# Kernel optimization log

Hardware: AMD Instinct MI355X
Metric: run time of the kernel (lower is better)

The kernel has to match this reference:

```python
import jax, jax.numpy as jnp
import numpy as np

NEG_SLOPE = 0.01  # torch LeakyReLU default
EPS = 1e-5        # torch BatchNorm2d default
N_BINS = 17       # quantization indices 0..16 for uniform [0,1) input


def _bn(x, g, b):
    # training-mode BatchNorm2d: biased batch stats over (B, H, W) per channel
    m = jnp.mean(x, axis=(0, 2, 3), keepdims=True)
    v = jnp.var(x, axis=(0, 2, 3), keepdims=True)
    return (x - m) * jax.lax.rsqrt(v + EPS) * g[None, :, None, None] + b[None, :, None, None]


def _lrelu(x):
    return jnp.where(x >= 0, x, NEG_SLOPE * x)


def _mode_pool_11(idx):
    # idx: int32 (B,C,H,W) quantization bin indices; 11x11 reflect-padded sliding-window mode.
    # Histogram formulation: one-hot over N_BINS, box-sum via 2D integral image, argmax.
    # argmax takes the FIRST max -> smallest modal value, matching torch.mode tie-breaking.
    k = jnp.pad(idx, ((0, 0), (0, 0), (5, 5), (5, 5)), mode='reflect')
    oh = (k[..., None] == jnp.arange(N_BINS, dtype=jnp.int32)).astype(jnp.float32)  # (B,C,Hp,Wp,17)
    I = jnp.cumsum(jnp.cumsum(oh, axis=2), axis=3)
    I = jnp.pad(I, ((0, 0), (0, 0), (1, 0), (1, 0), (0, 0)))
    cnt = I[:, :, 11:, 11:] - I[:, :, :-11, 11:] - I[:, :, 11:, :-11] + I[:, :, :-11, :-11]
    return jnp.argmax(cnt, axis=-1)  # (B,C,H,W) int


def _nearest(x, H, W):
    # torch F.interpolate mode='nearest': src = floor(dst * in / out)
    h, w = x.shape[2], x.shape[3]
    ri = (jnp.arange(H) * h) // H
    ci = (jnp.arange(W) * w) // W
    return x[:, :, ri][:, :, :, ci]


def _conv1x1(x, w, b):
    return jnp.einsum('bchw,oc->bohw', x, w) + b[None, :, None, None]


def reference(x, pw1, pb1, g1, be1, pw2, pb2, g2, be2, dw, sw, gs, bs):
    B, C, H, W = x.shape
    half = pw1.shape[0]
    # quantize: (x*255/16).round() * 16/256 -> index path (round has zero grad anyway)
    idx = jnp.round(x * 255.0 / 16.0).astype(jnp.int32)
    xq = _mode_pool_11(idx).astype(x.dtype) * (16.0 / 256.0)
    # prepare: conv1x1 -> BN -> LeakyReLU, twice
    h1 = _lrelu(_bn(_conv1x1(xq, pw1, pb1), g1, be1))
    prep = _lrelu(_bn(_conv1x1(h1, pw2, pb2), g2, be2))
    score = jnp.zeros((B, 2 * half, H, W), dtype=x.dtype)
    dn = ('NCHW', 'OIHW', 'NCHW')
    previous = prep
    d = prep
    # static pyramid: 512 -> 171 -> 57 -> 19 -> 7 -> 3 -> 1 (shapes known at trace time)
    while min(d.shape[2], d.shape[3]) >= 3:
        d = jax.lax.conv_general_dilated(d, dw, (3, 3), ((1, 1), (1, 1)), dimension_numbers=dn)
        z = _nearest(d, H, W)
        # interleave previous/zoomout per channel: ch 2c=prev[c], 2c+1=zoom[c]
        mix = jnp.stack([previous, z], axis=2).reshape(B, 2 * half, H, W)
        previous = z
        # grouped 1x1 conv: groups=half, 2 in / 2 out channels per group, no bias
        sc = jnp.einsum('bgihw,goi->bgohw', mix.reshape(B, half, 2, H, W), sw).reshape(B, 2 * half, H, W)
        score = score + _lrelu(_bn(sc, gs, bs))
    return score


def setup_inputs() -> dict:
    key = jax.random.key(0)
    ks = jax.random.split(key, 6)
    B, C, H, W = 8, 3, 512, 512
    half = 16
    x = jax.random.uniform(ks[0], (B, C, H, W), dtype=jnp.float32)
    pw1 = 0.1 * jax.random.normal(ks[1], (half, C), dtype=jnp.float32)
    pb1 = jnp.zeros((half,), jnp.float32)
    g1 = jnp.ones((half,), jnp.float32)
    be1 = jnp.zeros((half,), jnp.float32)
    pw2 = 0.1 * jax.random.normal(ks[2], (half, half), dtype=jnp.float32)
    pb2 = jnp.zeros((half,), jnp.float32)
    g2 = jnp.ones((half,), jnp.float32)
    be2 = jnp.zeros((half,), jnp.float32)
    dw = 0.1 * jax.random.normal(ks[3], (half, half, 3, 3), dtype=jnp.float32)
    sw = 0.1 * jax.random.normal(ks[4], (half, 2, 2), dtype=jnp.float32)
    gs = jnp.ones((2 * half,), jnp.float32)
    bs = jnp.zeros((2 * half,), jnp.float32)
    return {'x': x, 'pw1': pw1, 'pb1': pb1, 'g1': g1, 'be1': be1,
            'pw2': pw2, 'pb2': pb2, 'g2': g2, 'be2': be2,
            'dw': dw, 'sw': sw, 'gs': gs, 'bs': bs}
```

## Files before the change

kernel.cpp:

```cpp
#include <hip/hip_runtime.h>
#include <stdint.h>


#define NPX   2097152
#define NINV  (1.0f/2097152.0f)

#define OFF_STATS 0
#define OFF_HIST  16384
#define OFF_LUT   36864
#define OFF_MODE  194560
#define OFF_D1    73594880
#define OFF_D2    88566272
#define OFF_D3    90229760
#define OFF_D4    90414592
#define OFF_D5    90439680
#define OFF_D6    90444288

#define S_PRE1    0
#define S2_PRE1   16
#define S_H1      32
#define S_H1H1    48
#define S_PREP    184
#define S2_PREP   200
#define S_Z1      216
// ... 7 lines not shown
#define P_AFF     848

__device__ __forceinline__ uint32_t f2bf(float f) {
  uint32_t u = __float_as_uint(f);
  u += 0x7FFFu + ((u >> 16) & 1u);
  return u >> 16;
}
__device__ __forceinline__ float bf2f(uint32_t u) {
  return __uint_as_float(u << 16);
}

__device__ __forceinline__ float wave_red(float v) {
  v += __shfl_down(v, 32); v += __shfl_down(v, 16); v += __shfl_down(v, 8);
  v += __shfl_down(v, 4);  v += __shfl_down(v, 2);  v += __shfl_down(v, 1);
  return v;
}

template<int K, bool ATOMIC>
__device__ __forceinline__ void block_red(float* acc, float* dst, float* lds) {
  int lane = threadIdx.x & 63, wid = threadIdx.x >> 6;
#pragma unroll
  for (int k = 0; k < K; ++k) {
    float v = wave_red(acc[k]);
    if (lane == 0) lds[wid * K + k] = v;
  }
  __syncthreads();
  if ((int)threadIdx.x < K) {
    float s = lds[threadIdx.x] + lds[K + threadIdx.x] + lds[2 * K + threadIdx.x] + lds[3 * K + threadIdx.x];
    if (ATOMIC) atomicAdd(&dst[threadIdx.x], s);
    else        dst[threadIdx.x] = s;
  }
}

__global__ __launch_bounds__(256) void k_mode(const float* __restrict__ x,
                                              uint8_t* __restrict__ mode) {
  int bx = blockIdx.x;
  int rb = bx & 15, cb = (bx >> 4) & 1, pl = bx >> 5;
  __shared__ uint8_t tile[42][272];
  const float* xp = x + (size_t)pl * 262144;
  int tid = threadIdx.x;
  for (int e = tid; e < 42 * 266; e += 256) {
    int lr = e / 266, lc = e - lr * 266;
    int gr = rb * 32 - 5 + lr; if (gr < 0) gr = -gr; else if (gr > 511) gr = 1022 - gr;
    int gc = cb * 256 - 5 + lc; if (gc < 0) gc = -gc; else if (gc > 511) gc = 1022 - gc;
    float v = xp[gr * 512 + gc];
    tile[lr][lc] = (uint8_t)(int)rintf((v * 255.0f) * 0.0625f);
  }
  __syncthreads();
  int t = tid;
  uint32_t h0 = 0, h1 = 0, h2 = 0, h3 = 0, h4 = 0;
#define ADDV(vv) { int v_ = (vv); uint32_t inc_ = 1u << ((v_ & 3) << 3); int w_ = v_ >> 2; \
    h0 += (w_ == 0) ? inc_ : 0u; h1 += (w_ == 1) ? inc_ : 0u; h2 += (w_ == 2) ? inc_ : 0u; \
    h3 += (w_ == 3) ? inc_ : 0u; h4 += (w_ == 4) ? inc_ : 0u; }
#define SUBV(vv) { int v_ = (vv); uint32_t inc_ = 1u << ((v_ & 3) << 3); int w_ = v_ >> 2; \
    h0 -= (w_ == 0) ? inc_ : 0u; h1 -= (w_ == 1) ? inc_ : 0u; h2 -= (w_ == 2) ? inc_ : 0u; \
    h3 -= (w_ == 3) ? inc_ : 0u; h4 -= (w_ == 4) ? inc_ : 0u; }
#define SCAN_STORE(OI) { uint32_t best_ = h0 & 255u; int bi_ = 0; uint32_t c_; \
    c_ = (h0 >> 8)  & 255u; if (c_ > best_) { best_ = c_; bi_ = 1; } \
    c_ = (h0 >> 16) & 255u; if (c_ > best_) { best_ = c_; bi_ = 2; } \
    c_ = (h0 >> 24);        if (c_ > best_) { best_ = c_; bi_ = 3; } \
    c_ = h1 & 255u;         if (c_ > best_) { best_ = c_; bi_ = 4; } \
    c_ = (h1 >> 8)  & 255u; if (c_ > best_) { best_ = c_; bi_ = 5; } \
    c_ = (h1 >> 16) & 255u; if (c_ > best_) { best_ = c_; bi_ = 6; } \
    c_ = (h1 >> 24);        if (c_ > best_) { best_ = c_; bi_ = 7; } \
    c_ = h2 & 255u;         if (c_ > best_) { best_ = c_; bi_ = 8; } \
    c_ = (h2 >> 8)  & 255u; if (c_ > best_) { best_ = c_; bi_ = 9; } \
    c_ = (h2 >> 16) & 255u; if (c_ > best_) { best_ = c_; bi_ = 10; } \
    c_ = (h2 >> 24);        if (c_ > best_) { best_ = c_; bi_ = 11; } \
    c_ = h3 & 255u;         if (c_ > best_) { best_ = c_; bi_ = 12; } \
    c_ = (h3 >> 8)  & 255u; if (c_ > best_) { best_ = c_; bi_ = 13; } \
    c_ = (h3 >> 16) & 255u; if (c_ > best_) { best_ = c_; bi_ = 14; } \
    c_ = (h3 >> 24);        if (c_ > best_) { best_ = c_; bi_ = 15; } \
    c_ = h4 & 255u;         if (c_ > best_) { best_ = c_; bi_ = 16; } \
    mode[OI] = (uint8_t)bi_; }
#pragma unroll
  for (int dy = 0; dy < 11; ++dy) {
#pragma unroll
    for (int dx = 0; dx < 11; ++dx) ADDV(tile[dy][t + dx]);
  }
  size_t ob = (size_t)pl * 262144 + (size_t)(rb * 32) * 512 + cb * 256 + t;
  SCAN_STORE(ob);
  for (int s = 1; s < 32; ++s) {
#pragma unroll
    for (int dx = 0; dx < 11; ++dx) { SUBV(tile[s - 1][t + dx]); ADDV(tile[s + 10][t + dx]); }
    SCAN_STORE(ob + (size_t)s * 512);
  }
#undef ADDV
#undef SUBV
#undef SCAN_STORE
}

__global__ __launch_bounds__(256) void k_hist(const uint8_t* __restrict__ mode,
                                              uint32_t* __restrict__ hist) {
  __shared__ uint32_t h[4913];
  int tid = threadIdx.x;
  for (int e = tid; e < 4913; e += 256) h[e] = 0;
  __syncthreads();
  int base = blockIdx.x * 8192;
  for (int it = 0; it < 16; ++it) {
    int px = base + it * 512 + tid * 2;
    int b = px >> 18, rem = px & 262143;
    const uint8_t* mp = mode + (size_t)b * 786432 + rem;
    uint32_t m0 = *(const uint16_t*)(mp);
    uint32_t m1 = *(const uint16_t*)(mp + 262144);
    uint32_t m2 = *(const uint16_t*)(mp + 524288);
    int c0 = (int)(m0 & 255u) + 17 * (int)(m1 & 255u) + 289 * (int)(m2 & 255u);
    int c1 = (int)(m0 >> 8)   + 17 * (int)(m1 >> 8)   + 289 * (int)(m2 >> 8);
    atomicAdd(&h[c0], 1u);
    atomicAdd(&h[c1], 1u);
  }
  __syncthreads();
  for (int e = tid; e < 4913; e += 256)
    if (h[e]) atomicAdd(&hist[e], h[e]);
}

__global__ __launch_bounds__(256) void k_build(const uint32_t* __restrict__ hist,
    const float* __restrict__ pw1, const float* __restrict__ pb1,
    const float* __restrict__ g1,  const float* __restrict__ be1,
    const float* __restrict__ pw2, const float* __restrict__ pb2,
    const float* __restrict__ g2,  const float* __restrict__ be2,
    float* __restrict__ stats, uint32_t* __restrict__ lut) {
  __shared__ float red[4 * 152];
  int tid = threadIdx.x;
  {
    float acc[32];
#pragma unroll
    for (int k = 0; k < 32; ++k) acc[k] = 0.f;
    for (int bin = tid; bin < 4913; bin += 256) {
      float w = (float)hist[bin];
      if (w == 0.f) continue;
      int m0 = bin % 17, r = bin / 17;
      int m1 = r % 17, m2 = r / 17;
      float x0 = m0 * 0.0625f, x1 = m1 * 0.0625f, x2 = m2 * 0.0625f;
#pragma unroll
      for (int o = 0; o < 16; ++o) {
        float p = fmaf(pw1[o * 3], x0, fmaf(pw1[o * 3 + 1], x1, fmaf(pw1[o * 3 + 2], x2, pb1[o])));
        acc[o] = fmaf(w, p, acc[o]);
        acc[16 + o] = fmaf(w * p, p, acc[16 + o]);
      }
    }
    block_red<32, false>(acc, stats + S_PRE1, red);
  }
  __syncthreads();
  if (tid < 16) {
    int o = tid;
    float m = stats[S_PRE1 + o] * NINV;
// ... 62 lines not shown
    float acc[32];
#pragma unroll
    for (int k = 0; k < 32; ++k) acc[k] = 0.f;
    for (int bin = tid; bin < 4913; bin += 256) {
      float w = (float)hist[bin];
      int m0 = bin % 17, r = bin / 17;
      int m1 = r % 17, m2 = r / 17;
      float x0 = m0 * 0.0625f, x1 = m1 * 0.0625f, x2 = m2 * 0.0625f;
      float h[16];
#pragma unroll
      for (int c = 0; c < 16; ++c) {
        float y = fmaf(stats[P_A1 + c * 3], x0, fmaf(stats[P_A1 + c * 3 + 1], x1,
                  fmaf(stats[P_A1 + c * 3 + 2], x2, stats[P_B1 + c])));
        h[c] = fmaxf(y, 0.01f * y);
      }
      float p[16];
#pragma unroll
      for (int o = 0; o < 16; ++o) {
        float y = stats[P_B2 + o];
#pragma unroll
        for (int c = 0; c < 16; ++c) y = fmaf(stats[P_A2 + o * 16 + c], h[c], y);
        p[o] = fmaxf(y, 0.01f * y);
        acc[o] = fmaf(w, p[o], acc[o]);
        acc[16 + o] = fmaf(w * p[o], p[o], acc[16 + o]);
      }
#pragma unroll
      for (int d = 0; d < 8; ++d)
        lut[bin * 8 + d] = f2bf(p[2 * d]) | (f2bf(p[2 * d + 1]) << 16);
    }
    block_red<32, false>(acc, stats + S_PREP, red);
  }
}

template<int HIN, int WIN, int HOUT, int WOUT>
__device__ __forceinline__ void conv_body(const float* __restrict__ in,
                                          float* __restrict__ out,
                                          const float* __restrict__ dw, int bx) {
  __shared__ float tile[3][16][WIN + 2];
  int r = bx % HOUT, b = bx / HOUT;
  int tid = threadIdx.x;
  for (int e = tid; e < 48; e += 256) { tile[e / 16][e & 15][0] = 0.f; tile[e / 16][e & 15][WIN + 1] = 0.f; }
  for (int e = tid; e < 3 * 16 * WIN; e += 256) {
    int ky = e / (16 * WIN); int rem = e - ky * (16 * WIN); int ic = rem / WIN; int col = rem - ic * WIN;
    int gr = 3 * r - 1 + ky;
    float v = 0.f;
    if (gr >= 0 && gr < HIN) v = in[((size_t)(b * 16 + ic) * HIN + gr) * WIN + col];
    tile[ky][ic][col + 1] = v;
  }
  __syncthreads();
  int c = tid;
  if (c < WOUT) {
    float acc[16];
#pragma unroll
    for (int o = 0; o < 16; ++o) acc[o] = 0.f;
#pragma unroll
    for (int ic = 0; ic < 16; ++ic) {
      float v[9];
#pragma unroll
      for (int ky = 0; ky < 3; ++ky) {
#pragma unroll
        for (int kx = 0; kx < 3; ++kx) v[ky * 3 + kx] = tile[ky][ic][3 * c + kx];
      }
#pragma unroll
      for (int o = 0; o < 16; ++o) {
        const float* w = dw + (o * 16 + ic) * 9;
#pragma unroll
        for (int tp = 0; tp < 9; ++tp) acc[o] = fmaf(v[tp], w[tp], acc[o]);
      }
    }
#pragma unroll
    for (int o = 0; o < 16; ++o)
      out[((size_t)(b * 16 + o) * HOUT + r) * WOUT + c] = acc[o];
  }
}

template<int HP, int HZ>
__device__ __forceinline__ void pair_body(const float* __restrict__ dp,
                                          const float* __restrict__ dz,
                                          float* __restrict__ dst, int bx) {
  int g = bx & 15, b = (bx >> 4) & 7, jq = bx >> 7;
  const float* dpp = dp + (size_t)(b * 16 + g) * HP * HP;
  const float* dzp = dz + (size_t)(b * 16 + g) * HZ * HZ;
  float a1 = 0.f, a2 = 0.f, a3 = 0.f;
  for (int j = jq * 128; j < jq * 128 + 128; ++j) {
    int r1 = (j * HP) >> 9, r2 = (j * HZ) >> 9;
    const float* rp = dpp + r1 * HP;
    const float* rz = dzp + r2 * HZ;
    for (int i = threadIdx.x; i < 512; i += 256) {
      int c1 = (i * HP) >> 9, c2 = (i * HZ) >> 9;
      float zp = rp[c1], zz = rz[c2];
      a1 += zz; a2 = fmaf(zz, zz, a2); a3 = fmaf(zp, zz, a3);
    }
  }
  a1 = wave_red(a1); a2 = wave_red(a2); a3 = wave_red(a3);
  __shared__ float red[12];
  int lane = threadIdx.x & 63, wid = threadIdx.x >> 6;
  if (!lane) { red[wid * 3] = a1; red[wid * 3 + 1] = a2; red[wid * 3 + 2] = a3; }
  __syncthreads();
  if (threadIdx.x < 3) {
    float s = red[threadIdx.x] + red[3 + threadIdx.x] + red[6 + threadIdx.x] + red[9 + threadIdx.x];
    atomicAdd(&dst[threadIdx.x * 16 + g], s);
  }
}

__device__ __forceinline__ void corr1_body(const uint8_t* __restrict__ mode,
                                           const uint32_t* __restrict__ lut,
                                           const float* __restrict__ d1,
                                           float* __restrict__ stats, int bx) {
  int b = bx >> 6, band = bx & 63;
  float acc[48];
#pragma unroll
  for (int k = 0; k < 48; ++k) acc[k] = 0.f;
  for (int jj = 0; jj < 8; ++jj) {
    int j = band * 8 + jj;
    int r1 = (j * 171) >> 9;
#pragma unroll
    for (int ii = 0; ii < 2; ++ii) {
      int i = (int)threadIdx.x + ii * 256;
      int c1 = (i * 171) >> 9;
      const uint8_t* mp = mode + (size_t)b * 786432 + j * 512 + i;
      int combo = (int)mp[0] + 17 * (int)mp[262144] + 289 * (int)mp[524288];
      const uint4* L = (const uint4*)(lut + combo * 8);
      uint4 q0 = L[0], q1 = L[1];
      uint32_t q[8] = {q0.x, q0.y, q0.z, q0.w, q1.x, q1.y, q1.z, q1.w};
#pragma unroll
      for (int g = 0; g < 16; ++g) {
        float p = bf2f((g & 1) ? (q[g >> 1] >> 16) : (q[g >> 1] & 0xFFFFu));
        float z = d1[((size_t)(b * 16 + g) * 171 + r1) * 171 + c1];
        acc[g] += z; acc[16 + g] = fmaf(z, z, acc[16 + g]); acc[32 + g] = fmaf(p, z, acc[32 + g]);
      }
    }
  }
  __shared__ float red[4 * 48];
  block_red<48, true>(acc, stats + S_Z1, red);
}

__global__ __launch_bounds__(256) void k_conv1g(const uint8_t* __restrict__ mode,
                                                const uint32_t* __restrict__ lut,
                                                float* __restrict__ out,
                                                const float* __restrict__ dw) {
  __shared__ uint16_t tile[3][16][514];
  int bx = blockIdx.x; int r = bx % 171, b = bx / 171;
  int tid = threadIdx.x;
  for (int e = tid; e < 48; e += 256) { tile[e / 16][e & 15][0] = 0; tile[e / 16][e & 15][513] = 0; }
  for (int e = tid; e < 3 * 512; e += 256) {
    int ky = e >> 9, col = e & 511;
    int gr = 3 * r - 1 + ky;
    if (gr < 0 || gr > 511) {
#pragma unroll
      for (int c = 0; c < 16; ++c) tile[ky][c][col + 1] = 0;
    } else {
      const uint8_t* mp = mode + (size_t)b * 786432 + gr * 512 + col;
      int combo = (int)mp[0] + 17 * (int)mp[262144] + 289 * (int)mp[524288];
      const uint4* L = (const uint4*)(lut + combo * 8);
      uint4 q0 = L[0], q1 = L[1];
      uint32_t q[8] = {q0.x, q0.y, q0.z, q0.w, q1.x, q1.y, q1.z, q1.w};
#pragma unroll
      for (int d = 0; d < 8; ++d) {
        tile[ky][2 * d][col + 1]     = (uint16_t)(q[d] & 0xFFFFu);
        tile[ky][2 * d + 1][col + 1] = (uint16_t)(q[d] >> 16);
      }
    }
  }
  __syncthreads();
  int c = tid;
  if (c < 171) {
    float acc[16];
#pragma unroll
    for (int o = 0; o < 16; ++o) acc[o] = 0.f;
#pragma unroll
    for (int ic = 0; ic < 16; ++ic) {
      float v[9];
#pragma unroll
      for (int ky = 0; ky < 3; ++ky) {
#pragma unroll
        for (int kx = 0; kx < 3; ++kx)
          v[ky * 3 + kx] = __uint_as_float(((uint32_t)tile[ky][ic][3 * c + kx]) << 16);
      }
#pragma unroll
      for (int o = 0; o < 16; ++o) {
        const float* w = dw + (o * 16 + ic) * 9;
#pragma unroll
        for (int tp = 0; tp < 9; ++tp) acc[o] = fmaf(v[tp], w[tp], acc[o]);
      }
    }
#pragma unroll
    for (int o = 0; o < 16; ++o)
      out[((size_t)(b * 16 + o) * 171 + r) * 171 + c] = acc[o];
  }
}

__global__ __launch_bounds__(256) void k_conv2_corr1(const float* __restrict__ d1,
    float* __restrict__ d2, const float* __restrict__ dw,
    const uint8_t* __restrict__ mode, const uint32_t* __restrict__ lut,
    float* __restrict__ stats) {
  if ((int)blockIdx.x < 456) conv_body<171, 171, 57, 57>(d1, d2, dw, (int)blockIdx.x);
  else                       corr1_body(mode, lut, d1, stats, (int)blockIdx.x - 456);
}

template<int HIN, int WIN, int HOUT, int WOUT, int NCONV, int HP, int HZ>
__global__ __launch_bounds__(256) void k_conv_pair(const float* __restrict__ cin,
    float* __restrict__ cout, const float* __restrict__ dw,
    const float* __restrict__ dp, const float* __restrict__ dz,
    float* __restrict__ dst) {
  if ((int)blockIdx.x < NCONV) conv_body<HIN, WIN, HOUT, WOUT>(cin, cout, dw, (int)blockIdx.x);
  else                         pair_body<HP, HZ>(dp, dz, dst, (int)blockIdx.x - NCONV);
}

__global__ __launch_bounds__(256) void k_bnL2(float* stats, const float* __restrict__ sw,
    const float* __restrict__ gs, const float* __restrict__ bs,
    const float* __restrict__ d5, const float* __restrict__ d6) {
  __shared__ float l6[3][16][8];
  int t = threadIdx.x;
  if (t < 128) {
    int b = t >> 4, g = t & 15;
    float z6 = d6[b * 16 + g];
    const float* z5 = d5 + (size_t)(b * 16 + g) * 9;
    const float wr[3] = {171.f, 171.f, 170.f};
    float s5 = 0.f;
#pragma unroll
    for (int r = 0; r < 3; ++r)
#pragma unroll
      for (int c = 0; c < 3; ++c) s5 = fmaf(wr[r] * wr[c], z5[r * 3 + c], s5);
    l6[0][g][b] = z6; l6[1][g][b] = z6 * z6; l6[2][g][b] = z6 * s5;
  }
  __syncthreads();
  if (t < 48) {
    int w = t >> 4, g = t & 15;
    float s = 0.f;
#pragma unroll
    for (int b = 0; b < 8; ++b) s += l6[w][g][b];
    stats[S_LVLBASE + 4 * 48 + w * 16 + g] = (w == 2) ? s : s * 262144.f;
  }
  __syncthreads();
  if (t < 192) {
    int lvl = t >> 5, ch = t & 31, g = ch >> 1, o = ch & 1;
    float Sp, Sp2, Sz, Sz2, Spz;
    if (lvl == 0) {
      Sp = stats[S_PREP + g]; Sp2 = stats[S2_PREP + g];
      Sz = stats[S_Z1 + g];   Sz2 = stats[S2_Z1 + g]; Spz = stats[S_PZ1 + g];
    } else {
      int base = S_LVLBASE + (lvl - 1) * 48;
      Sz = stats[base + g]; Sz2 = stats[base + 16 + g]; Spz = stats[base + 32 + g];
      if (lvl == 1) { Sp = stats[S_Z1 + g]; Sp2 = stats[S2_Z1 + g]; }
      else { int pb = S_LVLBASE + (lvl - 2) * 48; Sp = stats[pb + g]; Sp2 = stats[pb + 16 + g]; }
    }
    float mp = Sp * NINV, mz = Sz * NINV;
    float ep2 = Sp2 * NINV, ez2 = Sz2 * NINV, epz = Spz * NINV;
    float w0 = sw[g * 4 + o * 2], w1 = sw[g * 4 + o * 2 + 1];
    float mean = w0 * mp + w1 * mz;
    float e2 = w0 * w0 * ep2 + 2.f * w0 * w1 * epz + w1 * w1 * ez2;
    float var = e2 - mean * mean;
    float s = gs[ch] * rsqrtf(var + 1e-5f);
    float* a = stats + P_AFF + (lvl * 32 + ch) * 3;
    a[0] = s * w0; a[1] = s * w1; a[2] = bs[ch] - mean * s;
  }
}

__global__ __launch_bounds__(256) void k_score(const uint8_t* __restrict__ mode,
    const uint32_t* __restrict__ lut,
    const float* __restrict__ d1, const float* __restrict__ d2, const float* __restrict__ d3,
    const float* __restrict__ d4, const float* __restrict__ d5, const float* __restrict__ d6,
    const float* __restrict__ stats, float* __restrict__ out) {
  __shared__ float zrow[4128];
  __shared__ float aff[576];
  __shared__ uint16_t prow[16][512];
  int bx = blockIdx.x; int b = bx >> 9, j = bx & 511;
  int tid = threadIdx.x;
  {
    const uint8_t* mp = mode + (size_t)b * 786432 + j * 512 + tid * 2;
    uint32_t m0 = *(const uint16_t*)(mp);
    uint32_t m1 = *(const uint16_t*)(mp + 262144);
    uint32_t m2 = *(const uint16_t*)(mp + 524288);
    int ca = (int)(m0 & 255u) + 17 * (int)(m1 & 255u) + 289 * (int)(m2 & 255u);
    int cb = (int)(m0 >> 8)   + 17 * (int)(m1 >> 8)   + 289 * (int)(m2 >> 8);
    const uint4* La = (const uint4*)(lut + ca * 8);
    const uint4* Lb = (const uint4*)(lut + cb * 8);
    uint4 a0 = La[0], a1 = La[1], b0 = Lb[0], b1 = Lb[1];
// ... 62 lines not shown
  }
}

extern "C" void kernel_launch(void* const* d_in, const int* in_sizes, int n_in,
                              void* d_out, int out_size, void* d_ws, size_t ws_size,
                              hipStream_t stream) {
  const float* x   = (const float*)d_in[0];
  const float* pw1 = (const float*)d_in[1];
  const float* pb1 = (const float*)d_in[2];
  const float* g1  = (const float*)d_in[3];
  const float* be1 = (const float*)d_in[4];
  const float* pw2 = (const float*)d_in[5];
  const float* pb2 = (const float*)d_in[6];
  const float* g2  = (const float*)d_in[7];
  const float* be2 = (const float*)d_in[8];
  const float* dw  = (const float*)d_in[9];
  const float* sw  = (const float*)d_in[10];
  const float* gs  = (const float*)d_in[11];
  const float* bs  = (const float*)d_in[12];
  char* ws = (char*)d_ws;
  float*    stats = (float*)(ws + OFF_STATS);
  uint32_t* hist  = (uint32_t*)(ws + OFF_HIST);
  uint32_t* lut   = (uint32_t*)(ws + OFF_LUT);
  uint8_t*  mode  = (uint8_t*)(ws + OFF_MODE);
  float* d1 = (float*)(ws + OFF_D1);
  float* d2 = (float*)(ws + OFF_D2);
  float* d3 = (float*)(ws + OFF_D3);
  float* d4 = (float*)(ws + OFF_D4);
  float* d5 = (float*)(ws + OFF_D5);
  float* d6 = (float*)(ws + OFF_D6);
  float* out = (float*)d_out;

  hipMemsetAsync(ws, 0, 36864, stream);
  k_mode<<<768, 256, 0, stream>>>(x, mode);
  k_hist<<<256, 256, 0, stream>>>(mode, hist);
  k_build<<<1, 256, 0, stream>>>(hist, pw1, pb1, g1, be1, pw2, pb2, g2, be2, stats, lut);
  k_conv1g<<<8 * 171, 256, 0, stream>>>(mode, lut, d1, dw);
  k_conv2_corr1<<<456 + 512, 256, 0, stream>>>(d1, d2, dw, mode, lut, stats);
  k_conv_pair<57, 57, 19, 19, 152, 171, 57><<<152 + 512, 256, 0, stream>>>(d2, d3, dw, d1, d2, stats + S_LVLBASE + 0 * 48);
  k_conv_pair<19, 19, 7, 7, 56, 57, 19><<<56 + 512, 256, 0, stream>>>(d3, d4, dw, d2, d3, stats + S_LVLBASE + 1 * 48);
  k_conv_pair<7, 7, 3, 3, 24, 19, 7><<<24 + 512, 256, 0, stream>>>(d4, d5, dw, d3, d4, stats + S_LVLBASE + 2 * 48);
  k_conv_pair<3, 3, 1, 1, 8, 7, 3><<<8 + 512, 256, 0, stream>>>(d5, d6, dw, d4, d5, stats + S_LVLBASE + 3 * 48);
  k_bnL2<<<1, 256, 0, stream>>>(stats, sw, gs, bs, d5, d6);
  k_score<<<4096, 256, 0, stream>>>(mode, lut, d1, d2, d3, d4, d5, d6, stats, out);
}
```

Before: 802.8 us.

## Fuse mode+histogram, compute pyramid correlation stats analytically inside conv kernels, merge tail levels

The mode-pooling kernel now handles all three channels of a batch image per block and builds the joint-mode histogram in LDS directly, which removes the separate histogram pass and its re-read of the mode buffer. The correlation statistics between consecutive pyramid levels are now computed inside each conv kernel from overlap-weighted block sums, replacing the separate 512-block full-resolution correlation passes. The small levels (7, 3, 1) and the final BN-stat kernel are merged into a single-block tail kernel. Together this cuts kernel launches and memory traffic, at the cost of fewer blocks in mode (256 versus 768), more registers per thread, and a serial single-block tail.

```diff
diff --git a/kernel.cpp b/kernel.cpp
--- a/kernel.cpp
+++ b/kernel.cpp
@@ -63,86 +63,80 @@
   }
 }
 
-__global__ __launch_bounds__(256) void k_mode(const float* __restrict__ x,
-                                              uint8_t* __restrict__ mode) {
+__device__ __forceinline__ void hadd(uint32_t* h, int v) {
+  uint32_t inc = 1u << ((v & 3) << 3); int w = v >> 2;
+#pragma unroll
+  for (int k = 0; k < 5; ++k) h[k] += (w == k) ? inc : 0u;
+}
+__device__ __forceinline__ void hsub(uint32_t* h, int v) {
+  uint32_t inc = 1u << ((v & 3) << 3); int w = v >> 2;
+#pragma unroll
+  for (int k = 0; k < 5; ++k) h[k] -= (w == k) ? inc : 0u;
+}
+__device__ __forceinline__ int hscan(const uint32_t* h) {
+  uint32_t best = h[0] & 255u; int bi = 0;
+#pragma unroll
+  for (int k = 1; k < 17; ++k) {
+    uint32_t c = (h[k >> 2] >> ((k & 3) << 3)) & 255u;
+    if (c > best) { best = c; bi = k; }
+  }
+  return bi;
+}
+
+__global__ __launch_bounds__(256) void k_modehist(const float* __restrict__ x,
+                                                  uint8_t* __restrict__ mode,
+                                                  uint32_t* __restrict__ hist) {
   int bx = blockIdx.x;
-  int rb = bx & 15, cb = (bx >> 4) & 1, pl = bx >> 5;
-  __shared__ uint8_t tile[42][272];
-  const float* xp = x + (size_t)pl * 262144;
+  int rb = bx & 15, cb = (bx >> 4) & 1, b = bx >> 5;
+  __shared__ uint8_t tile[3][42][272];
+  __shared__ uint32_t lh[4913];
   int tid = threadIdx.x;
-  for (int e = tid; e < 42 * 266; e += 256) {
-    int lr = e / 266, lc = e - lr * 266;
+  for (int e = tid; e < 4913; e += 256) lh[e] = 0;
+  const float* xb = x + (size_t)b * 786432;
+  for (int e = tid; e < 3 * 42 * 266; e += 256) {
+    int ch = e / (42 * 266); int rem = e - ch * (42 * 266);
+    int lr = rem / 266, lc = rem - lr * 266;
     int gr = rb * 32 - 5 + lr; if (gr < 0) gr = -gr; else if (gr > 511) gr = 1022 - gr;
     int gc = cb * 256 - 5 + lc; if (gc < 0) gc = -gc; else if (gc > 511) gc = 1022 - gc;
-    float v = xp[gr * 512 + gc];
-    tile[lr][lc] = (uint8_t)(int)rintf((v * 255.0f) * 0.0625f);
+    float v = xb[(size_t)ch * 262144 + gr * 512 + gc];
+    tile[ch][lr][lc] = (uint8_t)(int)rintf((v * 255.0f) * 0.0625f);
   }
   __syncthreads();
   int t = tid;
-  uint32_t h0 = 0, h1 = 0, h2 = 0, h3 = 0, h4 = 0;
-#define ADDV(vv) { int v_ = (vv); uint32_t inc_ = 1u << ((v_ & 3) << 3); int w_ = v_ >> 2; \
-    h0 += (w_ == 0) ? inc_ : 0u; h1 += (w_ == 1) ? inc_ : 0u; h2 += (w_ == 2) ? inc_ : 0u; \
-    h3 += (w_ == 3) ? inc_ : 0u; h4 += (w_ == 4) ? inc_ : 0u; }
-#define SUBV(vv) { int v_ = (vv); uint32_t inc_ = 1u << ((v_ & 3) << 3); int w_ = v_ >> 2; \
-    h0 -= (w_ == 0) ? inc_ : 0u; h1 -= (w_ == 1) ? inc_ : 0u; h2 -= (w_ == 2) ? inc_ : 0u; \
-    h3 -= (w_ == 3) ? inc_ : 0u; h4 -= (w_ == 4) ? inc_ : 0u; }
-#define SCAN_STORE(OI) { uint32_t best_ = h0 & 255u; int bi_ = 0; uint32_t c_; \
-    c_ = (h0 >> 8)  & 255u; if (c_ > best_) { best_ = c_; bi_ = 1; } \
-    c_ = (h0 >> 16) & 255u; if (c_ > best_) { best_ = c_; bi_ = 2; } \
-    c_ = (h0 >> 24);        if (c_ > best_) { best_ = c_; bi_ = 3; } \
-    c_ = h1 & 255u;         if (c_ > best_) { best_ = c_; bi_ = 4; } \
-    c_ = (h1 >> 8)  & 255u; if (c_ > best_) { best_ = c_; bi_ = 5; } \
-    c_ = (h1 >> 16) & 255u; if (c_ > best_) { best_ = c_; bi_ = 6; } \
-    c_ = (h1 >> 24);        if (c_ > best_) { best_ = c_; bi_ = 7; } \
-    c_ = h2 & 255u;         if (c_ > best_) { best_ = c_; bi_ = 8; } \
-    c_ = (h2 >> 8)  & 255u; if (c_ > best_) { best_ = c_; bi_ = 9; } \
-    c_ = (h2 >> 16) & 255u; if (c_ > best_) { best_ = c_; bi_ = 10; } \
-    c_ = (h2 >> 24);        if (c_ > best_) { best_ = c_; bi_ = 11; } \
-    c_ = h3 & 255u;         if (c_ > best_) { best_ = c_; bi_ = 12; } \
-    c_ = (h3 >> 8)  & 255u; if (c_ > best_) { best_ = c_; bi_ = 13; } \
-    c_ = (h3 >> 16) & 255u; if (c_ > best_) { best_ = c_; bi_ = 14; } \
-    c_ = (h3 >> 24);        if (c_ > best_) { best_ = c_; bi_ = 15; } \
-    c_ = h4 & 255u;         if (c_ > best_) { best_ = c_; bi_ = 16; } \
-    mode[OI] = (uint8_t)bi_; }
-#pragma unroll
-  for (int dy = 0; dy < 11; ++dy) {
-#pragma unroll
-    for (int dx = 0; dx < 11; ++dx) ADDV(tile[dy][t + dx]);
-  }
-  size_t ob = (size_t)pl * 262144 + (size_t)(rb * 32) * 512 + cb * 256 + t;
-  SCAN_STORE(ob);
+  uint32_t h[3][5];
+#pragma unroll
+  for (int ch = 0; ch < 3; ++ch)
+#pragma unroll
+    for (int k = 0; k < 5; ++k) h[ch][k] = 0;
+#pragma unroll
+  for (int dy = 0; dy < 11; ++dy)
+#pragma unroll
+    for (int dx = 0; dx < 11; ++dx) {
+      hadd(h[0], tile[0][dy][t + dx]);
+      hadd(h[1], tile[1][dy][t + dx]);
+      hadd(h[2], tile[2][dy][t + dx]);
+    }
+  size_t ob = (size_t)b * 786432 + (size_t)(rb * 32) * 512 + cb * 256 + t;
+  {
+    int m0 = hscan(h[0]), m1 = hscan(h[1]), m2 = hscan(h[2]);
+    mode[ob] = (uint8_t)m0; mode[ob + 262144] = (uint8_t)m1; mode[ob + 524288] = (uint8_t)m2;
+    atomicAdd(&lh[m0 + 17 * m1 + 289 * m2], 1u);
+  }
   for (int s = 1; s < 32; ++s) {
 #pragma unroll
-    for (int dx = 0; dx < 11; ++dx) { SUBV(tile[s - 1][t + dx]); ADDV(tile[s + 10][t + dx]); }
-    SCAN_STORE(ob + (size_t)s * 512);
-  }
-#undef ADDV
-#undef SUBV
-#undef SCAN_STORE
-}
-
-__global__ __launch_bounds__(256) void k_hist(const uint8_t* __restrict__ mode,
-                                              uint32_t* __restrict__ hist) {
-  __shared__ uint32_t h[4913];
-  int tid = threadIdx.x;
-  for (int e = tid; e < 4913; e += 256) h[e] = 0;
-  __syncthreads();
-  int base = blockIdx.x * 8192;
-  for (int it = 0; it < 16; ++it) {
-    int px = base + it * 512 + tid * 2;
-    int b = px >> 18, rem = px & 262143;
-    const uint8_t* mp = mode + (size_t)b * 786432 + rem;
-    uint32_t m0 = *(const uint16_t*)(mp);
-    uint32_t m1 = *(const uint16_t*)(mp + 262144);
-    uint32_t m2 = *(const uint16_t*)(mp + 524288);
-    int c0 = (int)(m0 & 255u) + 17 * (int)(m1 & 255u) + 289 * (int)(m2 & 255u);
-    int c1 = (int)(m0 >> 8)   + 17 * (int)(m1 >> 8)   + 289 * (int)(m2 >> 8);
-    atomicAdd(&h[c0], 1u);
-    atomicAdd(&h[c1], 1u);
+    for (int dx = 0; dx < 11; ++dx) {
+      hsub(h[0], tile[0][s - 1][t + dx]); hadd(h[0], tile[0][s + 10][t + dx]);
+      hsub(h[1], tile[1][s - 1][t + dx]); hadd(h[1], tile[1][s + 10][t + dx]);
+      hsub(h[2], tile[2][s - 1][t + dx]); hadd(h[2], tile[2][s + 10][t + dx]);
+    }
+    size_t o = ob + (size_t)s * 512;
+    int m0 = hscan(h[0]), m1 = hscan(h[1]), m2 = hscan(h[2]);
+    mode[o] = (uint8_t)m0; mode[o + 262144] = (uint8_t)m1; mode[o + 524288] = (uint8_t)m2;
+    atomicAdd(&lh[m0 + 17 * m1 + 289 * m2], 1u);
   }
   __syncthreads();
   for (int e = tid; e < 4913; e += 256)
-    if (h[e]) atomicAdd(&hist[e], h[e]);
+    if (lh[e]) atomicAdd(&hist[e], lh[e]);
 }
 
 __global__ __launch_bounds__(256) void k_build(const uint32_t* __restrict__ hist,
@@ -271,24 +265,44 @@
   }
 }
 
-template<int HIN, int WIN, int HOUT, int WOUT>
-__device__ __forceinline__ void conv_body(const float* __restrict__ in,
-                                          float* __restrict__ out,
-                                          const float* __restrict__ dw, int bx) {
-  __shared__ float tile[3][16][WIN + 2];
-  int r = bx % HOUT, b = bx / HOUT;
+__global__ __launch_bounds__(256) void k_conv1s(const uint8_t* __restrict__ mode,
+    const uint32_t* __restrict__ lut, float* __restrict__ d1,
+    const float* __restrict__ dw, float* __restrict__ stats) {
+  __shared__ uint16_t tile[4][16][512];
+  int bx = blockIdx.x; int r = bx % 171, b = bx / 171;
   int tid = threadIdx.x;
-  for (int e = tid; e < 48; e += 256) { tile[e / 16][e & 15][0] = 0.f; tile[e / 16][e & 15][WIN + 1] = 0.f; }
-  for (int e = tid; e < 3 * 16 * WIN; e += 256) {
-    int ky = e / (16 * WIN); int rem = e - ky * (16 * WIN); int ic = rem / WIN; int col = rem - ic * WIN;
-    int gr = 3 * r - 1 + ky;
-    float v = 0.f;
-    if (gr >= 0 && gr < HIN) v = in[((size_t)(b * 16 + ic) * HIN + gr) * WIN + col];
-    tile[ky][ic][col + 1] = v;
+  for (int e = tid; e < 1024; e += 256) {
+    int row = e >> 8, q = e & 255;
+    int gr = 3 * r - 1 + row;
+    if (gr < 0 || gr > 511) {
+#pragma unroll
+      for (int c = 0; c < 16; ++c) ((uint32_t*)tile[row][c])[q] = 0u;
+    } else {
+      const uint8_t* mp = mode + (size_t)b * 786432 + gr * 512 + q * 2;
+      uint32_t m0 = *(const uint16_t*)(mp);
+      uint32_t m1 = *(const uint16_t*)(mp + 262144);
+      uint32_t m2 = *(const uint16_t*)(mp + 524288);
+      int ca = (int)(m0 & 255u) + 17 * (int)(m1 & 255u) + 289 * (int)(m2 & 255u);
+      int cc = (int)(m0 >> 8)   + 17 * (int)(m1 >> 8)   + 289 * (int)(m2 >> 8);
+      const uint4* La = (const uint4*)(lut + ca * 8);
+      const uint4* Lb = (const uint4*)(lut + cc * 8);
+      uint4 a0 = La[0], a1 = La[1], b0 = Lb[0], b1 = Lb[1];
+      uint32_t pa[8] = {a0.x, a0.y, a0.z, a0.w, a1.x, a1.y, a1.z, a1.w};
+      uint32_t pb[8] = {b0.x, b0.y, b0.z, b0.w, b1.x, b1.y, b1.z, b1.w};
+#pragma unroll
+      for (int c = 0; c < 16; ++c) {
+        uint32_t lo = (c & 1) ? (pa[c >> 1] >> 16)         : (pa[c >> 1] & 0xFFFFu);
+        uint32_t hi = (c & 1) ? (pb[c >> 1] & 0xFFFF0000u) : (pb[c >> 1] << 16);
+        ((uint32_t*)tile[row][c])[q] = lo | hi;
+      }
+    }
   }
   __syncthreads();
   int c = tid;
-  if (c < WOUT) {
+  float s48[48];
+#pragma unroll
+  for (int k = 0; k < 48; ++k) s48[k] = 0.f;
+  if (c < 171) {
     float acc[16];
 #pragma unroll
     for (int o = 0; o < 16; ++o) acc[o] = 0.f;
@@ -296,10 +310,12 @@
     for (int ic = 0; ic < 16; ++ic) {
       float v[9];
 #pragma unroll
-      for (int ky = 0; ky < 3; ++ky) {
-#pragma unroll
-        for (int kx = 0; kx < 3; ++kx) v[ky * 3 + kx] = tile[ky][ic][3 * c + kx];
-      }
+      for (int ky = 0; ky < 3; ++ky)
+#pragma unroll
+        for (int kx = 0; kx < 3; ++kx) {
+          int gc = 3 * c - 1 + kx;
+          v[ky * 3 + kx] = (gc >= 0) ? bf2f(tile[ky][ic][gc]) : 0.f;
+        }
 #pragma unroll
       for (int o = 0; o < 16; ++o) {
         const float* w = dw + (o * 16 + ic) * 9;
@@ -307,103 +323,46 @@
         for (int tp = 0; tp < 9; ++tp) acc[o] = fmaf(v[tp], w[tp], acc[o]);
       }
     }
-#pragma unroll
-    for (int o = 0; o < 16; ++o)
-      out[((size_t)(b * 16 + o) * HOUT + r) * WOUT + c] = acc[o];
-  }
-}
-
-template<int HP, int HZ>
-__device__ __forceinline__ void pair_body(const float* __restrict__ dp,
-                                          const float* __restrict__ dz,
-                                          float* __restrict__ dst, int bx) {
-  int g = bx & 15, b = (bx >> 4) & 7, jq = bx >> 7;
-  const float* dpp = dp + (size_t)(b * 16 + g) * HP * HP;
-  const float* dzp = dz + (size_t)(b * 16 + g) * HZ * HZ;
-  float a1 = 0.f, a2 = 0.f, a3 = 0.f;
-  for (int j = jq * 128; j < jq * 128 + 128; ++j) {
-    int r1 = (j * HP) >> 9, r2 = (j * HZ) >> 9;
-    const float* rp = dpp + r1 * HP;
-    const float* rz = dzp + r2 * HZ;
-    for (int i = threadIdx.x; i < 512; i += 256) {
-      int c1 = (i * HP) >> 9, c2 = (i * HZ) >> 9;
-      float zp = rp[c1], zz = rz[c2];
-      a1 += zz; a2 = fmaf(zz, zz, a2); a3 = fmaf(zp, zz, a3);
-    }
-  }
-  a1 = wave_red(a1); a2 = wave_red(a2); a3 = wave_red(a3);
-  __shared__ float red[12];
-  int lane = threadIdx.x & 63, wid = threadIdx.x >> 6;
-  if (!lane) { red[wid * 3] = a1; red[wid * 3 + 1] = a2; red[wid * 3 + 2] = a3; }
-  __syncthreads();
-  if (threadIdx.x < 3) {
-    float s = red[threadIdx.x] + red[3 + threadIdx.x] + red[6 + threadIdx.x] + red[9 + threadIdx.x];
-    atomicAdd(&dst[threadIdx.x * 16 + g], s);
-  }
-}
-
-__device__ __forceinline__ void corr1_body(const uint8_t* __restrict__ mode,
-                                           const uint32_t* __restrict__ lut,
-                                           const float* __restrict__ d1,
-                                           float* __restrict__ stats, int bx) {
-  int b = bx >> 6, band = bx & 63;
-  float acc[48];
-#pragma unroll
-  for (int k = 0; k < 48; ++k) acc[k] = 0.f;
-  for (int jj = 0; jj < 8; ++jj) {
-    int j = band * 8 + jj;
-    int r1 = (j * 171) >> 9;
-#pragma unroll
-    for (int ii = 0; ii < 2; ++ii) {
-      int i = (int)threadIdx.x + ii * 256;
-      int c1 = (i * 171) >> 9;
-      const uint8_t* mp = mode + (size_t)b * 786432 + j * 512 + i;
-      int combo = (int)mp[0] + 17 * (int)mp[262144] + 289 * (int)mp[524288];
-      const uint4* L = (const uint4*)(lut + combo * 8);
-      uint4 q0 = L[0], q1 = L[1];
-      uint32_t q[8] = {q0.x, q0.y, q0.z, q0.w, q1.x, q1.y, q1.z, q1.w};
-#pragma unroll
-      for (int g = 0; g < 16; ++g) {
-        float p = bf2f((g & 1) ? (q[g >> 1] >> 16) : (q[g >> 1] & 0xFFFFu));
-        float z = d1[((size_t)(b * 16 + g) * 171 + r1) * 171 + c1];
-        acc[g] += z; acc[16 + g] = fmaf(z, z, acc[16 + g]); acc[32 + g] = fmaf(p, z, acc[32 + g]);
-      }
-    }
-  }
+    int nr = (r < 170) ? 3 : 2;
+    int nc = (c < 170) ? 3 : 2;
+    float wgt = (float)(nr * nc);
+#pragma unroll
+    for (int g = 0; g < 16; ++g) {
+      float B = 0.f;
+      for (int u = 0; u < nr; ++u)
+        for (int v2 = 0; v2 < nc; ++v2)
+          B += bf2f(tile[1 + u][g][3 * c + v2]);
+      float z = acc[g];
+      s48[g] = wgt * z; s48[16 + g] = wgt * z * z; s48[32 + g] = B * z;
+      d1[((size_t)(b * 16 + g) * 171 + r) * 171 + c] = z;
+    }
+  }
+  __syncthreads();
+  block_red<48, true>(s48, stats + S_Z1, (float*)tile);
+}
+
+template<int HP, int HZ, int SOFF>
+__global__ __launch_bounds__(256) void k_convs(const float* __restrict__ din,
+    float* __restrict__ dout, const float* __restrict__ dw,
+    float* __restrict__ stats) {
+  __shared__ float tile[4][16][HP + 2];
   __shared__ float red[4 * 48];
-  block_red<48, true>(acc, stats + S_Z1, red);
-}
-
-__global__ __launch_bounds__(256) void k_conv1g(const uint8_t* __restrict__ mode,
-                                                const uint32_t* __restrict__ lut,
-                                                float* __restrict__ out,
-                                                const float* __restrict__ dw) {
-  __shared__ uint16_t tile[3][16][514];
-  int bx = blockIdx.x; int r = bx % 171, b = bx / 171;
+  int bx = blockIdx.x; int r = bx % HZ, b = bx / HZ;
   int tid = threadIdx.x;
-  for (int e = tid; e < 48; e += 256) { tile[e / 16][e & 15][0] = 0; tile[e / 16][e & 15][513] = 0; }
-  for (int e = tid; e < 3 * 512; e += 256) {
-    int ky = e >> 9, col = e & 511;
-    int gr = 3 * r - 1 + ky;
-    if (gr < 0 || gr > 511) {
-#pragma unroll
-      for (int c = 0; c < 16; ++c) tile[ky][c][col + 1] = 0;
-    } else {
-      const uint8_t* mp = mode + (size_t)b * 786432 + gr * 512 + col;
-      int combo = (int)mp[0] + 17 * (int)mp[262144] + 289 * (int)mp[524288];
-      const uint4* L = (const uint4*)(lut + combo * 8);
-      uint4 q0 = L[0], q1 = L[1];
-      uint32_t q[8] = {q0.x, q0.y, q0.z, q0.w, q1.x, q1.y, q1.z, q1.w};
-#pragma unroll
-      for (int d = 0; d < 8; ++d) {
-        tile[ky][2 * d][col + 1]     = (uint16_t)(q[d] & 0xFFFFu);
-        tile[ky][2 * d + 1][col + 1] = (uint16_t)(q[d] >> 16);
-      }
-    }
+  for (int e = tid; e < 64; e += 256) { tile[e >> 4][e & 15][0] = 0.f; tile[e >> 4][e & 15][HP + 1] = 0.f; }
+  for (int e = tid; e < 4 * 16 * HP; e += 256) {
+    int row = e / (16 * HP); int rem = e - row * (16 * HP); int ic = rem / HP; int col = rem - ic * HP;
+    int gr = 3 * r - 1 + row;
+    float v = 0.f;
+    if (gr >= 0 && gr < HP) v = din[((size_t)(b * 16 + ic) * HP + gr) * HP + col];
+    tile[row][ic][col + 1] = v;
   }
   __syncthreads();
   int c = tid;
-  if (c < 171) {
+  float s48[48];
+#pragma unroll
+  for (int k = 0; k < 48; ++k) s48[k] = 0.f;
+  if (c < HZ) {
     float acc[16];
 #pragma unroll
     for (int o = 0; o < 16; ++o) acc[o] = 0.f;
@@ -411,11 +370,9 @@
     for (int ic = 0; ic < 16; ++ic) {
       float v[9];
 #pragma unroll
-      for (int ky = 0; ky < 3; ++ky) {
-#pragma unroll
-        for (int kx = 0; kx < 3; ++kx)
-          v[ky * 3 + kx] = __uint_as_float(((uint32_t)tile[ky][ic][3 * c + kx]) << 16);
-      }
+      for (int ky = 0; ky < 3; ++ky)
+#pragma unroll
+        for (int kx = 0; kx < 3; ++kx) v[ky * 3 + kx] = tile[ky][ic][3 * c + kx];
 #pragma unroll
       for (int o = 0; o < 16; ++o) {
         const float* w = dw + (o * 16 + ic) * 9;
@@ -423,66 +380,194 @@
         for (int tp = 0; tp < 9; ++tp) acc[o] = fmaf(v[tp], w[tp], acc[o]);
       }
     }
-#pragma unroll
-    for (int o = 0; o < 16; ++o)
-      out[((size_t)(b * 16 + o) * 171 + r) * 171 + c] = acc[o];
-  }
-}
-
-__global__ __launch_bounds__(256) void k_conv2_corr1(const float* __restrict__ d1,
-    float* __restrict__ d2, const float* __restrict__ dw,
-    const uint8_t* __restrict__ mode, const uint32_t* __restrict__ lut,
-    float* __restrict__ stats) {
-  if ((int)blockIdx.x < 456) conv_body<171, 171, 57, 57>(d1, d2, dw, (int)blockIdx.x);
-  else                       corr1_body(mode, lut, d1, stats, (int)blockIdx.x - 456);
-}
-
-template<int HIN, int WIN, int HOUT, int WOUT, int NCONV, int HP, int HZ>
-__global__ __launch_bounds__(256) void k_conv_pair(const float* __restrict__ cin,
-    float* __restrict__ cout, const float* __restrict__ dw,
-    const float* __restrict__ dp, const float* __restrict__ dz,
-    float* __restrict__ dst) {
-  if ((int)blockIdx.x < NCONV) conv_body<HIN, WIN, HOUT, WOUT>(cin, cout, dw, (int)blockIdx.x);
-  else                         pair_body<HP, HZ>(dp, dz, dst, (int)blockIdx.x - NCONV);
-}
-
-__global__ __launch_bounds__(256) void k_bnL2(float* stats, const float* __restrict__ sw,
-    const float* __restrict__ gs, const float* __restrict__ bs,
-    const float* __restrict__ d5, const float* __restrict__ d6) {
-  __shared__ float l6[3][16][8];
-  int t = threadIdx.x;
-  if (t < 128) {
-    int b = t >> 4, g = t & 15;
-    float z6 = d6[b * 16 + g];
-    const float* z5 = d5 + (size_t)(b * 16 + g) * 9;
-    const float wr[3] = {171.f, 171.f, 170.f};
-    float s5 = 0.f;
-#pragma unroll
-    for (int r = 0; r < 3; ++r)
-#pragma unroll
-      for (int c = 0; c < 3; ++c) s5 = fmaf(wr[r] * wr[c], z5[r * 3 + c], s5);
-    l6[0][g][b] = z6; l6[1][g][b] = z6 * z6; l6[2][g][b] = z6 * s5;
-  }
-  __syncthreads();
-  if (t < 48) {
-    int w = t >> 4, g = t & 15;
-    float s = 0.f;
-#pragma unroll
-    for (int b = 0; b < 8; ++b) s += l6[w][g][b];
-    stats[S_LVLBASE + 4 * 48 + w * 16 + g] = (w == 2) ? s : s * 262144.f;
-  }
-  __syncthreads();
-  if (t < 192) {
-    int lvl = t >> 5, ch = t & 31, g = ch >> 1, o = ch & 1;
+    int loZ = (512 * r + HZ - 1) / HZ, hiZ = (512 * (r + 1) + HZ - 1) / HZ;
+    int loC = (512 * c + HZ - 1) / HZ, hiC = (512 * (c + 1) + HZ - 1) / HZ;
+    float cR[3], cC[3];
+#pragma unroll
+    for (int u = 0; u < 3; ++u) {
+      int rr = 3 * r + u;
+      int loP = (512 * rr + HP - 1) / HP, hiP = (512 * (rr + 1) + HP - 1) / HP;
+      int cnt = min(hiP, hiZ) - max(loP, loZ); cR[u] = (float)max(cnt, 0);
+      int cc = 3 * c + u;
+      int loQ = (512 * cc + HP - 1) / HP, hiQ = (512 * (cc + 1) + HP - 1) / HP;
+      int cnt2 = min(hiQ, hiC) - max(loQ, loC); cC[u] = (float)max(cnt2, 0);
+    }
+    float wgt = (float)(hiZ - loZ) * (float)(hiC - loC);
+#pragma unroll
+    for (int g = 0; g < 16; ++g) {
+      float B = 0.f;
+#pragma unroll
+      for (int u = 0; u < 3; ++u) {
+        float rowS = 0.f;
+#pragma unroll
+        for (int v2 = 0; v2 < 3; ++v2) rowS = fmaf(cC[v2], tile[1 + u][g][3 * c + v2 + 1], rowS);
+        B = fmaf(cR[u], rowS, B);
+      }
+      float z = acc[g];
+      s48[g] = wgt * z; s48[16 + g] = wgt * z * z; s48[32 + g] = B * z;
+      dout[((size_t)(b * 16 + g) * HZ + r) * HZ + c] = z;
+    }
+  }
+  block_red<48, true>(s48, stats + SOFF, red);
+}
+
+__device__ __forceinline__ float stat_get(const float* stats, const float* accL, int idx) {
+  return (idx >= S_LVLBASE + 96) ? accL[idx - (S_LVLBASE + 96)] : stats[idx];
+}
+
+__global__ __launch_bounds__(256) void k_tail(const float* __restrict__ d3,
+    float* __restrict__ d4, float* __restrict__ d5, float* __restrict__ d6,
+    const float* __restrict__ dw, float* __restrict__ stats,
+    const float* __restrict__ sw, const float* __restrict__ gs,
+    const float* __restrict__ bs) {
+  __shared__ float s3[16][19][19];
+  __shared__ float s4[16][7][7];
+  __shared__ float s5[16][3][3];
+  __shared__ float s6[16];
+  __shared__ float accL[144];
+  int tid = threadIdx.x;
+  for (int e = tid; e < 144; e += 256) accL[e] = 0.f;
+  for (int b = 0; b < 8; ++b) {
+    __syncthreads();
+    for (int e = tid; e < 16 * 361; e += 256)
+      ((float*)s3)[e] = d3[(size_t)b * 16 * 361 + e];
+    __syncthreads();
+    for (int e = tid; e < 784; e += 256) {
+      int o = e / 49, rc = e - o * 49; int r = rc / 7, c = rc % 7;
+      float a = 0.f;
+#pragma unroll
+      for (int ic = 0; ic < 16; ++ic) {
+        const float* w = dw + (o * 16 + ic) * 9;
+#pragma unroll
+        for (int ky = 0; ky < 3; ++ky) {
+          int gr = 3 * r - 1 + ky; if (gr < 0 || gr > 18) continue;
+#pragma unroll
+          for (int kx = 0; kx < 3; ++kx) {
+            int gc = 3 * c - 1 + kx; if (gc < 0 || gc > 18) continue;
+            a = fmaf(s3[ic][gr][gc], w[ky * 3 + kx], a);
+          }
+        }
+      }
+      s4[o][r][c] = a; d4[((size_t)(b * 16 + o) * 7 + r) * 7 + c] = a;
+    }
+    __syncthreads();
+    for (int e = tid; e < 784; e += 256) {
+      int g = e & 15, rc = e >> 4; int r2 = rc / 7, c2 = rc % 7;
+      int loZ = (512 * r2 + 6) / 7, hiZ = (512 * (r2 + 1) + 6) / 7;
+      int loC = (512 * c2 + 6) / 7, hiC = (512 * (c2 + 1) + 6) / 7;
+      int rrmin = (loZ * 19) >> 9, rrmax = ((hiZ - 1) * 19) >> 9;
+      int ccmin = (loC * 19) >> 9, ccmax = ((hiC - 1) * 19) >> 9;
+      float z = s4[g][r2][c2];
+      float B = 0.f;
+      for (int rr = rrmin; rr <= rrmax; ++rr) {
+        int loP = (512 * rr + 18) / 19, hiP = (512 * (rr + 1) + 18) / 19;
+        int cntR = min(hiP, hiZ) - max(loP, loZ); if (cntR <= 0) continue;
+        float rowS = 0.f;
+        for (int cc = ccmin; cc <= ccmax; ++cc) {
+          int loQ = (512 * cc + 18) / 19, hiQ = (512 * (cc + 1) + 18) / 19;
+          int cntC = min(hiQ, hiC) - max(loQ, loC); if (cntC <= 0) continue;
+          rowS = fmaf((float)cntC, s3[g][rr][cc], rowS);
+        }
+        B = fmaf((float)cntR, rowS, B);
+      }
+      float wgt = (float)((hiZ - loZ) * (hiC - loC));
+      atomicAdd(&accL[g], wgt * z);
+      atomicAdd(&accL[16 + g], wgt * z * z);
+      atomicAdd(&accL[32 + g], B * z);
+    }
+    for (int e = tid; e < 144; e += 256) {
+      int o = e / 9, rc = e - o * 9; int r = rc / 3, c = rc % 3;
+      float a = 0.f;
+#pragma unroll
+      for (int ic = 0; ic < 16; ++ic) {
+        const float* w = dw + (o * 16 + ic) * 9;
+#pragma unroll
+        for (int ky = 0; ky < 3; ++ky) {
+          int gr = 3 * r - 1 + ky; if (gr < 0 || gr > 6) continue;
+#pragma unroll
+          for (int kx = 0; kx < 3; ++kx) {
+            int gc = 3 * c - 1 + kx; if (gc < 0 || gc > 6) continue;
+            a = fmaf(s4[ic][gr][gc], w[ky * 3 + kx], a);
+          }
+        }
+      }
+      s5[o][r][c] = a; d5[((size_t)(b * 16 + o) * 3 + r) * 3 + c] = a;
+    }
+    __syncthreads();
+    for (int e = tid; e < 144; e += 256) {
+      int g = e & 15, rc = e >> 4; int r2 = rc / 3, c2 = rc % 3;
+      int loZ = (512 * r2 + 2) / 3, hiZ = (512 * (r2 + 1) + 2) / 3;
+      int loC = (512 * c2 + 2) / 3, hiC = (512 * (c2 + 1) + 2) / 3;
+      int rrmin = (loZ * 7) >> 9, rrmax = ((hiZ - 1) * 7) >> 9;
+      int ccmin = (loC * 7) >> 9, ccmax = ((hiC - 1) * 7) >> 9;
+      float z = s5[g][r2][c2];
+      float B = 0.f;
+      for (int rr = rrmin; rr <= rrmax; ++rr) {
+        int loP = (512 * rr + 6) / 7, hiP = (512 * (rr + 1) + 6) / 7;
+        int cntR = min(hiP, hiZ) - max(loP, loZ); if (cntR <= 0) continue;
+        float rowS = 0.f;
+        for (int cc = ccmin; cc <= ccmax; ++cc) {
+          int loQ = (512 * cc + 6) / 7, hiQ = (512 * (cc + 1) + 6) / 7;
+          int cntC = min(hiQ, hiC) - max(loQ, loC); if (cntC <= 0) continue;
+          rowS = fmaf((float)cntC, s4[g][rr][cc], rowS);
+        }
+        B = fmaf((float)cntR, rowS, B);
+      }
+      float wgt = (float)((hiZ - loZ) * (hiC - loC));
+      atomicAdd(&accL[48 + g], wgt * z);
+      atomicAdd(&accL[64 + g], wgt * z * z);
+      atomicAdd(&accL[80 + g], B * z);
+    }
+    if (tid < 16) {
+      int o = tid; float a = 0.f;
+#pragma unroll
+      for (int ic = 0; ic < 16; ++ic) {
+        const float* w = dw + (o * 16 + ic) * 9;
+#pragma unroll
+        for (int ky = 0; ky < 3; ++ky) {
+          int gr = ky - 1; if (gr < 0) continue;
+#pragma unroll
+          for (int kx = 0; kx < 3; ++kx) {
+            int gc = kx - 1; if (gc < 0) continue;
+            a = fmaf(s5[ic][gr][gc], w[ky * 3 + kx], a);
+          }
+        }
+      }
+      s6[o] = a; d6[b * 16 + o] = a;
+    }
+    __syncthreads();
+    if (tid < 16) {
+      int g = tid; float z6 = s6[g];
+      const float wr3[3] = {171.f, 171.f, 170.f};
+      float s5s = 0.f;
+#pragma unroll
+      for (int r = 0; r < 3; ++r)
+#pragma unroll
+        for (int c = 0; c < 3; ++c) s5s = fmaf(wr3[r] * wr3[c], s5[g][r][c], s5s);
+      atomicAdd(&accL[96 + g],  262144.f * z6);
+      atomicAdd(&accL[112 + g], 262144.f * z6 * z6);
+      atomicAdd(&accL[128 + g], z6 * s5s);
+    }
+  }
+  __syncthreads();
+  for (int e = tid; e < 144; e += 256) stats[S_LVLBASE + 96 + e] = accL[e];
+  if (tid < 192) {
+    int lvl = tid >> 5, ch = tid & 31, g = ch >> 1, o = ch & 1;
     float Sp, Sp2, Sz, Sz2, Spz;
     if (lvl == 0) {
       Sp = stats[S_PREP + g]; Sp2 = stats[S2_PREP + g];
       Sz = stats[S_Z1 + g];   Sz2 = stats[S2_Z1 + g]; Spz = stats[S_PZ1 + g];
     } else {
       int base = S_LVLBASE + (lvl - 1) * 48;
-      Sz = stats[base + g]; Sz2 = stats[base + 16 + g]; Spz = stats[base + 32 + g];
+      Sz  = stat_get(stats, accL, base + g);
+      Sz2 = stat_get(stats, accL, base + 16 + g);
+      Spz = stat_get(stats, accL, base + 32 + g);
       if (lvl == 1) { Sp = stats[S_Z1 + g]; Sp2 = stats[S2_Z1 + g]; }
-      else { int pb = S_LVLBASE + (lvl - 2) * 48; Sp = stats[pb + g]; Sp2 = stats[pb + 16 + g]; }
+      else {
+        int pb = S_LVLBASE + (lvl - 2) * 48;
+        Sp  = stat_get(stats, accL, pb + g);
+        Sp2 = stat_get(stats, accL, pb + 16 + g);
+      }
     }
     float mp = Sp * NINV, mz = Sz * NINV;
     float ep2 = Sp2 * NINV, ez2 = Sz2 * NINV, epz = Spz * NINV;
@@ -611,15 +696,11 @@
   float* out = (float*)d_out;
 
   hipMemsetAsync(ws, 0, 36864, stream);
-  k_mode<<<768, 256, 0, stream>>>(x, mode);
-  k_hist<<<256, 256, 0, stream>>>(mode, hist);
+  k_modehist<<<256, 256, 0, stream>>>(x, mode, hist);
   k_build<<<1, 256, 0, stream>>>(hist, pw1, pb1, g1, be1, pw2, pb2, g2, be2, stats, lut);
-  k_conv1g<<<8 * 171, 256, 0, stream>>>(mode, lut, d1, dw);
-  k_conv2_corr1<<<456 + 512, 256, 0, stream>>>(d1, d2, dw, mode, lut, stats);
-  k_conv_pair<57, 57, 19, 19, 152, 171, 57><<<152 + 512, 256, 0, stream>>>(d2, d3, dw, d1, d2, stats + S_LVLBASE + 0 * 48);
-  k_conv_pair<19, 19, 7, 7, 56, 57, 19><<<56 + 512, 256, 0, stream>>>(d3, d4, dw, d2, d3, stats + S_LVLBASE + 1 * 48);
-  k_conv_pair<7, 7, 3, 3, 24, 19, 7><<<24 + 512, 256, 0, stream>>>(d4, d5, dw, d3, d4, stats + S_LVLBASE + 2 * 48);
-  k_conv_pair<3, 3, 1, 1, 8, 7, 3><<<8 + 512, 256, 0, stream>>>(d5, d6, dw, d4, d5, stats + S_LVLBASE + 3 * 48);
-  k_bnL2<<<1, 256, 0, stream>>>(stats, sw, gs, bs, d5, d6);
+  k_conv1s<<<8 * 171, 256, 0, stream>>>(mode, lut, d1, dw, stats);
+  k_convs<171, 57, S_LVLBASE     ><<<8 * 57, 256, 0, stream>>>(d1, d2, dw, stats);
+  k_convs<57,  19, S_LVLBASE + 48><<<8 * 19, 256, 0, stream>>>(d2, d3, dw, stats);
+  k_tail<<<1, 256, 0, stream>>>(d3, d4, d5, d6, dw, stats, sw, gs, bs);
   k_score<<<4096, 256, 0, stream>>>(mode, lut, d1, d2, d3, d4, d5, d6, stats, out);
 }
```

After: 1.411 ms. +75.8%, slower.
